# Optimization experiments

Hardware: AMD Instinct MI355X
Metric: run time of the kernel (lower is better)

## Reference

```python
import jax, jax.numpy as jnp
import numpy as np

N = 50000      # nodes (single node type 'tx')
E = 400000     # edges per edge type ('fwd' and 'rev')
F_IN = 128     # input feature dim
F = 128        # cfg.gnn.dim_inner
H = 8          # attention heads
D = F // H     # per-head dim
L = 2          # cfg.gnn.layers_mp
C = 2          # dim_out (fraud logits)


def setup_inputs() -> dict:
    key = jax.random.key(0)
    k = jax.random.split(key, 12)
    f32 = jnp.float32
    g = lambda kk, sh, fan: jax.random.normal(kk, sh, f32) / np.float32(np.sqrt(fan))
    return dict(
        x=jax.random.normal(k[0], (N, F_IN), f32),
        edge_index_fwd=jax.random.randint(k[1], (2, E), 0, N),
        edge_index_rev=jax.random.randint(k[2], (2, E), 0, N),
        in_w=g(k[3], (F_IN, F), F_IN),
        in_b=jnp.zeros((F,), f32),
        kqv_w=g(k[4], (L, F, 3 * F), F),
        kqv_b=jnp.zeros((L, 3 * F), f32),
        krel_w=g(k[5], (L, 2, H, D, D), D),
        vrel_w=g(k[6], (L, 2, H, D, D), D),
        p_rel=jnp.ones((L, 2, H), f32),
        out_w=g(k[7], (L, F, F), F),
        out_b=jnp.zeros((L, F), f32),
        skip=jnp.ones((L,), f32),
        head_w=g(k[8], (F, C), F),
        head_b=jnp.zeros((C,), f32),
    )


def reference(x, edge_index_fwd, edge_index_rev, in_w, in_b, kqv_w, kqv_b,
              krel_w, vrel_w, p_rel, out_w, out_b, skip, head_w, head_b):
    n = x.shape[0]
    ef, er = edge_index_fwd, edge_index_rev
    Ef, Er = ef.shape[1], er.shape[1]
    dst = jnp.concatenate([ef[1], er[1]])                 # [E_tot]
    scale = 1.0 / jnp.sqrt(jnp.asarray(D, x.dtype))

    h = x @ in_w + in_b                                   # in_proj['tx'], [N,F]
    for l in range(L):
        kqv = h @ kqv_w[l] + kqv_b[l]                     # [N,3F]
        k, q, v = jnp.split(kqv, 3, axis=1)
        k = k.reshape(n, H, D)
        q = q.reshape(n, H, D)
        v = v.reshape(n, H, D)
        # per-edge-type relation transforms (head-wise DxD, no bias)
        k_rel = jnp.einsum('nhd,ehdf->enhf', k, krel_w[l])  # [2,N,H,D]
        v_rel = jnp.einsum('nhd,ehdf->enhf', v, vrel_w[l])
        # gather src features per edge type, concatenate edge types
        k_j = jnp.concatenate([k_rel[0][ef[0]], k_rel[1][er[0]]], axis=0)  # [E_tot,H,D]
        v_j = jnp.concatenate([v_rel[0][ef[0]], v_rel[1][er[0]]], axis=0)
        p_e = jnp.concatenate([jnp.broadcast_to(p_rel[l, 0], (Ef, H)),
                               jnp.broadcast_to(p_rel[l, 1], (Er, H))], axis=0)
        q_i = q[dst]                                       # [E_tot,H,D]
        alpha = jnp.einsum('ehd,ehd->eh', q_i, k_j) * p_e * scale
        # segment softmax over all incoming edges of each dst node
        m = jax.ops.segment_max(alpha, dst, num_segments=n)
        ex = jnp.exp(alpha - m[dst])
        denom = jax.ops.segment_sum(ex, dst, num_segments=n)
        w = ex / (denom[dst] + 1e-16)                      # [E_tot,H]
        agg = jax.ops.segment_sum(w[:, :, None] * v_j, dst,
                                  num_segments=n).reshape(n, F)
        a = jax.nn.gelu(agg, approximate=False) @ out_w[l] + out_b[l]
        g = jax.nn.sigmoid(skip[l])
        h = jax.nn.relu(g * a + (1.0 - g) * h)             # skip + act(dropout=0)
    return h @ head_w + head_b                             # logits [N,C]
```

## Files before the change

kernel.cpp:

```cpp
#include <hip/hip_runtime.h>
#include <math.h>

typedef short short8 __attribute__((ext_vector_type(8)));
typedef float f32x4 __attribute__((ext_vector_type(4)));

#define CAP 64
#define CSTR 16

__device__ __forceinline__ unsigned short f2bf(float f){
    unsigned u = __float_as_uint(f);
    unsigned r = u + 0x7fffu + ((u >> 16) & 1u);
    return (unsigned short)(r >> 16);
}
__device__ __forceinline__ float bf2f(unsigned short s){
    return __uint_as_float((unsigned)s << 16);
}

__global__ void k_setup(const float* __restrict__ kqv_w, const float* __restrict__ kqv_b,
                        const float* __restrict__ krel_w, const float* __restrict__ vrel_w,
                        const float* __restrict__ p_rel, const float* __restrict__ out_w,
                        const float* __restrict__ out_b, const float* __restrict__ in_w,
                        const float* __restrict__ x, const float* __restrict__ head_b,
                        const int* __restrict__ ef, const int* __restrict__ er,
                        unsigned short* __restrict__ WcT, float* __restrict__ biasc,
                        unsigned short* __restrict__ WoT, float* __restrict__ biaso,
                        unsigned short* __restrict__ WiT, unsigned short* __restrict__ x16,
                        int* __restrict__ cnt, unsigned* __restrict__ srcs_pad,
                        float* __restrict__ logits, int n_nodes, int Ef, int Er)
{
    const long long E0 = Ef + Er;
    const long long N0 = E0 + 2*129*640;
    const long long N1 = N0 + 2*129*128;
    const long long N2 = N1 + 128*128;
    const long long N3 = N2 + (long long)n_nodes*32;
    const long long N4 = N3 + 2*n_nodes;

    for (long long idx = (long long)blockIdx.x*blockDim.x + threadIdx.x; idx < N4;
         idx += (long long)gridDim.x*blockDim.x) {
        if (idx < E0) {
            int e = (int)idx;
            int src, dst, tt;
            if (e < Ef) { src = ef[e]; dst = ef[Ef + e]; tt = 0; }
            else { int e2 = e - Ef; src = er[e2]; dst = er[Er + e2]; tt = 1; }
            int pos = atomicAdd(&cnt[(size_t)dst*CSTR], 1);
            if (pos < CAP)
                srcs_pad[dst*CAP + pos] = (unsigned)(tt*n_nodes + src)*32u;
        } else if (idx < N0) {
            int i = (int)(idx - E0);
            int l = i / (129*640);
            int rem = i % (129*640);
            int r = rem / 640, c = rem % 640;
            float val;
            if (c < 128) {
                val = (r < 128) ? kqv_w[((size_t)l*128 + r)*384 + 128 + c]
                                : kqv_b[l*384 + 128 + c];
            } else {
                int c2 = c - 128;
                int tt = c2 >> 8;
                int cc = c2 & 255;
                int f = cc >> 1;
                int part = cc & 1;
                int hh = f >> 4, fd = f & 15;
                const float* rw = (part == 0 ? krel_w : vrel_w)
                                  + (((size_t)(l*2 + tt)*8 + hh)*16)*16 + fd;
                int base_col = (part == 0 ? 0 : 256) + hh*16;
                float s = 0.f;
                #pragma unroll
                for (int d = 0; d < 16; ++d) {
                    float a = (r < 128) ? kqv_w[((size_t)l*128 + r)*384 + base_col + d]
                                        : kqv_b[l*384 + base_col + d];
                    s += a * rw[d*16];
                }
                if (part == 0) s *= p_rel[(l*2 + tt)*8 + hh] * 0.25f * 1.4426950408889634f;
                val = s;
            }
            if (r < 128) WcT[((size_t)l*640 + c)*128 + r] = f2bf(val);
            else         biasc[l*640 + c] = val;
        } else if (idx < N1) {
            int i = (int)(idx - N0);
            int l = i / (129*128);
            int rem = i % (129*128);
            int r = rem / 128, c = rem % 128;
            if (r < 128) WoT[((size_t)l*128 + c)*128 + r] = f2bf(out_w[((size_t)l*128 + r)*128 + c]);
            else         biaso[l*128 + c] = out_b[l*128 + c];
        } else if (idx < N2) {
            int i = (int)(idx - N1);
            int r = i >> 7, c = i & 127;
            WiT[(size_t)c*128 + r] = f2bf(in_w[(size_t)r*128 + c]);
        } else if (idx < N3) {
            long long i = idx - N2;
            float4 v = *(const float4*)&x[i*4];
            uint2 w;
            w.x = (unsigned)f2bf(v.x) | ((unsigned)f2bf(v.y) << 16);
            w.y = (unsigned)f2bf(v.z) | ((unsigned)f2bf(v.w) << 16);
            *(uint2*)&x16[i*4] = w;
        } else {
            long long i = idx - N3;
            logits[i] = head_b[i & 1];
        }
    }
}

__global__ __launch_bounds__(256) void k_mfma(
    const unsigned short* __restrict__ A16, const unsigned short* __restrict__ WT,
    const float* __restrict__ biasc, unsigned short* __restrict__ q16,
    unsigned short* __restrict__ h16, unsigned* __restrict__ kv,
    const float* __restrict__ skip, const float* __restrict__ hw,
    float* __restrict__ logits, int l,
    int n_nodes, int R, int C, int mode)
{
    __shared__ uint4 As[64*16];
    __shared__ uint4 Ws[64*16];
    int b = blockIdx.x;
    int xcd = b & 7, jj = b >> 3;
    int r_t = (jj / C)*8 + xcd;
    int c_t = jj % C;
    if (r_t >= R) return;
    int n0 = r_t*64, c0 = c_t*64;
    int t = threadIdx.x;

    #pragma unroll
    for (int it = 0; it < 4; ++it) {
        int gi = t + it*256;
        int m = gi >> 4, g = gi & 15;
        uint4 a = *(const uint4*)&A16[((size_t)(n0 + m)*16 + g)*8];
        As[m*16 + (g ^ (m & 15))] = a;
    }
    #pragma unroll
    for (int it = 0; it < 4; ++it) {
        int gi = t + it*256;
        int cw = gi >> 4, g = gi & 15;
        uint4 wv = *(const uint4*)&WT[((size_t)(c0 + cw)*16 + g)*8];
        Ws[cw*16 + (g ^ (cw & 15))] = wv;
    }
    __syncthreads();

    int lane = t & 63, w = t >> 6;
    int lm = lane & 15, quad = lane >> 4;
    f32x4 acc[4];
    #pragma unroll
    for (int i = 0; i < 4; ++i) { acc[i][0]=0.f; acc[i][1]=0.f; acc[i][2]=0.f; acc[i][3]=0.f; }

    #pragma unroll
    for (int chunk = 0; chunk < 4; ++chunk) {
        int gq = chunk*4 + quad;
        short8 bfrag = *(const short8*)&Ws[(w*16 + lm)*16 + (gq ^ lm)];
        #pragma unroll
        for (int i = 0; i < 4; ++i) {
            short8 afrag = *(const short8*)&As[(i*16 + lm)*16 + (gq ^ lm)];
            acc[i] = __builtin_amdgcn_mfma_f32_16x16x32_bf16(afrag, bfrag, acc[i], 0, 0, 0);
        }
    }

    int c = c0 + w*16 + lm;
    float bc = biasc[c];
    bool even = (lane & 1) == 0;
    if (mode == 3) {
        float g = 1.f/(1.f + expf(-skip[l]));
        float hw0 = hw[c*2], hw1 = hw[c*2 + 1];
        #pragma unroll
        for (int i = 0; i < 4; ++i) {
            #pragma unroll
            for (int rr = 0; rr < 4; ++rr) {
                int m = n0 + i*16 + quad*4 + rr;
                float nv = 0.f;
                if (m < n_nodes) {
                    float hv = bf2f(h16[(size_t)m*128 + c]);
                    nv = fmaxf(g*(acc[i][rr] + bc) + (1.f - g)*hv, 0.f);
                }
                float p0 = nv*hw0, p1 = nv*hw1;
                p0 += __shfl_xor(p0, 1); p1 += __shfl_xor(p1, 1);
                p0 += __shfl_xor(p0, 2); p1 += __shfl_xor(p1, 2);
                p0 += __shfl_xor(p0, 4); p1 += __shfl_xor(p1, 4);
                p0 += __shfl_xor(p0, 8); p1 += __shfl_xor(p1, 8);
                if (lm == 0 && m < n_nodes) {
                    atomicAdd(&logits[m*2],     p0);
                    atomicAdd(&logits[m*2 + 1], p1);
                }
            }
        }
    } else if (mode == 2) {
        float g = 1.f/(1.f + expf(-skip[l]));
        unsigned* dst = (unsigned*)h16;
        #pragma unroll
        for (int i = 0; i < 4; ++i) {
            #pragma unroll
            for (int rr = 0; rr < 4; ++rr) {
                int m = n0 + i*16 + quad*4 + rr;
                float hv = (m < n_nodes) ? bf2f(h16[(size_t)m*128 + c]) : 0.f;
                float nv = fmaxf(g*(acc[i][rr] + bc) + (1.f - g)*hv, 0.f);
                float other = __shfl_xor(nv, 1);
                if (even && m < n_nodes)
                    dst[(size_t)m*64 + (c >> 1)] =
                        (unsigned)f2bf(nv) | ((unsigned)f2bf(other) << 16);
            }
        }
    } else if (mode == 0) {
        unsigned* dst = (unsigned*)h16;
        #pragma unroll
        for (int i = 0; i < 4; ++i) {
            #pragma unroll
            for (int rr = 0; rr < 4; ++rr) {
                int m = n0 + i*16 + quad*4 + rr;
                float nv = acc[i][rr] + bc;
                float other = __shfl_xor(nv, 1);
                if (even && m < n_nodes)
                    dst[(size_t)m*64 + (c >> 1)] =
                        (unsigned)f2bf(nv) | ((unsigned)f2bf(other) << 16);
            }
        }
    } else if (c0 < 128) {
        unsigned* dst = (unsigned*)q16;
        #pragma unroll
        for (int i = 0; i < 4; ++i) {
            #pragma unroll
            for (int rr = 0; rr < 4; ++rr) {
                float val = acc[i][rr] + bc;
                float other = __shfl_xor(val, 1);
                int m = n0 + i*16 + quad*4 + rr;
                if (even && m < n_nodes)
                    dst[(size_t)m*64 + (c >> 1)] =
                        (unsigned)f2bf(val) | ((unsigned)f2bf(other) << 16);
            }
        }
    } else {
        int c2 = c - 128;
        int tt = c2 >> 8;
        int f = (c2 & 255) >> 1;
        unsigned* dst = kv + (size_t)tt*n_nodes*128;
        #pragma unroll
        for (int i = 0; i < 4; ++i) {
            #pragma unroll
            for (int rr = 0; rr < 4; ++rr) {
                float val = acc[i][rr] + bc;
                float other = __shfl_xor(val, 1);
                int m = n0 + i*16 + quad*4 + rr;
                if (even && m < n_nodes) {
                    unsigned wd = ((unsigned)f2bf(val) << 16) | (unsigned)f2bf(other);
                    dst[(size_t)m*128 + f] = wd;
                }
            }
        }
    }
}

__global__ __launch_bounds__(256) void k_attn(
    const unsigned* __restrict__ srcs_pad, const int* __restrict__ cnt,
    const uint4* __restrict__ kv, const unsigned short* __restrict__ q16,
    unsigned short* __restrict__ qa16, int n_base, int n_hi)
{
    int lane = threadIdx.x & 31;
    int n = n_base + blockIdx.x*8 + (threadIdx.x >> 5);
    if (n >= n_hi) return;
    uint2 qp = *(const uint2*)&q16[(size_t)n*128 + lane*4];
    float4 q4;
    q4.x = __uint_as_float(qp.x << 16);
    q4.y = __uint_as_float(qp.x & 0xffff0000u);
    q4.z = __uint_as_float(qp.y << 16);
    q4.w = __uint_as_float(qp.y & 0xffff0000u);
    int s = n*CAP, e = s + min(cnt[(size_t)n*CSTR], CAP);

    const uint4* kvl = kv + lane;
    const unsigned* srcs = srcs_pad;

    float lsum = 0.f;
    float4 a = make_float4(0.f, 0.f, 0.f, 0.f);

    unsigned sv0 = srcs[s],     sv1 = srcs[s + 1];
    unsigned sv2 = srcs[s + 2], sv3 = srcs[s + 3];
    uint4 w0 = kvl[sv0], w1 = kvl[sv1], w2 = kvl[sv2], w3 = kvl[sv3];

    int pos = s;

#define ATT_PAIR(wA, wB)                                                       \
    {                                                                          \
        float d0 = __uint_as_float(wA.x & 0xffff0000u)*q4.x                    \
                 + __uint_as_float(wA.y & 0xffff0000u)*q4.y                    \
                 + __uint_as_float(wA.z & 0xffff0000u)*q4.z                    \
                 + __uint_as_float(wA.w & 0xffff0000u)*q4.w;                   \
        float d1 = __uint_as_float(wB.x & 0xffff0000u)*q4.x                    \
                 + __uint_as_float(wB.y & 0xffff0000u)*q4.y                    \
                 + __uint_as_float(wB.z & 0xffff0000u)*q4.z                    \
                 + __uint_as_float(wB.w & 0xffff0000u)*q4.w;                   \
        d0 += __shfl_xor(d0, 1); d1 += __shfl_xor(d1, 1);                      \
        d0 += __shfl_xor(d0, 2); d1 += __shfl_xor(d1, 2);                      \
        float wt0 = exp2f(d0), wt1 = exp2f(d1);                                \
        lsum += wt0 + wt1;                                                     \
        a.x += wt0*__uint_as_float(wA.x << 16);                                \
        a.y += wt0*__uint_as_float(wA.y << 16);                                \
        a.z += wt0*__uint_as_float(wA.z << 16);                                \
        a.w += wt0*__uint_as_float(wA.w << 16);                                \
        a.x += wt1*__uint_as_float(wB.x << 16);                                \
        a.y += wt1*__uint_as_float(wB.y << 16);                                \
        a.z += wt1*__uint_as_float(wB.z << 16);                                \
        a.w += wt1*__uint_as_float(wB.w << 16);                                \
    }

#define ATT_ONE(wA)                                                            \
    {                                                                          \
        float d = __uint_as_float(wA.x & 0xffff0000u)*q4.x                     \
                + __uint_as_float(wA.y & 0xffff0000u)*q4.y                     \
                + __uint_as_float(wA.z & 0xffff0000u)*q4.z                     \
                + __uint_as_float(wA.w & 0xffff0000u)*q4.w;                    \
        d += __shfl_xor(d, 1);                                                 \
        d += __shfl_xor(d, 2);                                                 \
        float wt = exp2f(d);                                                   \
        lsum += wt;                                                            \
        a.x += wt*__uint_as_float(wA.x << 16);                                 \
        a.y += wt*__uint_as_float(wA.y << 16);                                 \
        a.z += wt*__uint_as_float(wA.z << 16);                                 \
        a.w += wt*__uint_as_float(wA.w << 16);                                 \
    }

    for (; pos + 3 < e; pos += 4) {
        unsigned p0 = srcs[pos + 4], p1 = srcs[pos + 5];
        ATT_PAIR(w0, w1);
        w0 = kvl[p0]; w1 = kvl[p1];
        unsigned p2 = srcs[pos + 6], p3 = srcs[pos + 7];
        ATT_PAIR(w2, w3);
        w2 = kvl[p2]; w3 = kvl[p3];
    }
    int rem = e - pos;
    if (rem > 0) {
        ATT_ONE(w0);
        if (rem > 1) ATT_ONE(w1);
        if (rem > 2) ATT_ONE(w2);
    }
#undef ATT_PAIR
#undef ATT_ONE

    float inv = 1.f/(lsum + 1e-16f);
    float x0 = a.x*inv, x1 = a.y*inv, x2 = a.z*inv, x3 = a.w*inv;
    float g0 = 0.5f*x0*(1.f + erff(x0*0.70710678118654752f));
    float g1 = 0.5f*x1*(1.f + erff(x1*0.70710678118654752f));
    float g2 = 0.5f*x2*(1.f + erff(x2*0.70710678118654752f));
    float g3 = 0.5f*x3*(1.f + erff(x3*0.70710678118654752f));
    uint2 pk;
    pk.x = (unsigned)f2bf(g0) | ((unsigned)f2bf(g1) << 16);
    pk.y = (unsigned)f2bf(g2) | ((unsigned)f2bf(g3) << 16);
    *(uint2*)&qa16[(size_t)n*128 + lane*4] = pk;
}

extern "C" void kernel_launch(void* const* d_in, const int* in_sizes, int n_in,
                              void* d_out, int out_size, void* d_ws, size_t ws_size,
                              hipStream_t stream)
{
    const float* x      = (const float*)d_in[0];
    const int*   ef     = (const int*)d_in[1];
    const int*   er     = (const int*)d_in[2];
    const float* in_w   = (const float*)d_in[3];
    const float* in_b   = (const float*)d_in[4];
    const float* kqv_w  = (const float*)d_in[5];
    const float* kqv_b  = (const float*)d_in[6];
    const float* krel_w = (const float*)d_in[7];
    const float* vrel_w = (const float*)d_in[8];
    const float* p_rel  = (const float*)d_in[9];
    const float* out_w  = (const float*)d_in[10];
    const float* out_b  = (const float*)d_in[11];
    const float* skip   = (const float*)d_in[12];
    const float* head_w = (const float*)d_in[13];
    const float* head_b = (const float*)d_in[14];
    float* out = (float*)d_out;

    int n_nodes = in_sizes[0] / 128;
    int Ef = in_sizes[1] / 2, Er = in_sizes[2] / 2;
    int ntile = (n_nodes + 63)/64;
    int npad = ntile*64;

    float* p = (float*)d_ws;
    unsigned* kv = (unsigned*)p; p += (size_t)2*n_nodes*128;
    unsigned short* h16  = (unsigned short*)p; p += (size_t)npad*128/2;
    unsigned short* q16  = (unsigned short*)p; p += (size_t)npad*128/2;
    unsigned short* qa16 = (unsigned short*)p; p += (size_t)npad*128/2;
    unsigned short* x16  = (unsigned short*)p; p += (size_t)npad*128/2;
    unsigned short* WiT = (unsigned short*)p; p += (size_t)(128*128)/2;
    unsigned short* WcT = (unsigned short*)p; p += (size_t)(2*640*128)/2;
    float* biasc = p; p += 2*640;
    unsigned short* WoT = (unsigned short*)p; p += (size_t)(2*128*128)/2;
    float* biaso = p; p += 2*128;
    int* cnt = (int*)p;            p += (size_t)n_nodes*CSTR;
    unsigned* srcs_pad = (unsigned*)p; p += (size_t)n_nodes*CAP;

    int Rg = (ntile + 7)/8;

    hipMemsetAsync(cnt, 0, (size_t)n_nodes*CSTR*sizeof(int), stream);
    hipMemsetAsync(srcs_pad, 0, (size_t)n_nodes*CAP*sizeof(unsigned), stream);
    k_setup<<<7500, 256, 0, stream>>>(kqv_w, kqv_b, krel_w, vrel_w, p_rel, out_w, out_b,
                                      in_w, x, head_b, ef, er, WcT, biasc, WoT, biaso,
                                      WiT, x16, cnt, srcs_pad, out, n_nodes, Ef, Er);

    int nh = (((n_nodes + 1)/2) + 7) & ~7;
    if (nh > n_nodes) nh = n_nodes;

    k_mfma<<<Rg*8*2, 256, 0, stream>>>(x16, WiT, in_b, nullptr, h16, kv, skip,
                                       head_w, out, 0, n_nodes, ntile, 2, 0);
    for (int l = 0; l < 2; ++l) {
        k_mfma<<<Rg*8*10, 256, 0, stream>>>(h16, WcT + (size_t)l*640*128,
                                            biasc + l*640, q16, nullptr, kv, skip,
                                            head_w, out, l, n_nodes, ntile, 10, 1);
        k_attn<<<nh/8, 256, 0, stream>>>(srcs_pad, cnt, (const uint4*)kv, q16, qa16,
                                         0, nh);
        k_attn<<<(n_nodes - nh + 7)/8, 256, 0, stream>>>(srcs_pad, cnt, (const uint4*)kv,
                                                         q16, qa16, nh, n_nodes);
        int omode = (l == 1) ? 3 : 2;
        k_mfma<<<Rg*8*2, 256, 0, stream>>>(qa16, WoT + (size_t)l*128*128,
                                           biaso + l*128, nullptr, h16, kv, skip,
                                           head_w, out, l, n_nodes, ntile, 2, omode);
    }
}
```

Baseline: 394.5 us.

## Partition edge bucketing by XCD so each die handles its own destination range

```diff
diff --git a/kernel.cpp b/kernel.cpp
--- a/kernel.cpp
+++ b/kernel.cpp
@@ -6,6 +6,7 @@
 
 #define CAP 64
 #define CSTR 16
+#define ECHUNK 2048
 
 __device__ __forceinline__ unsigned short f2bf(float f){
     unsigned u = __float_as_uint(f);
@@ -26,10 +27,38 @@
                         unsigned short* __restrict__ WoT, float* __restrict__ biaso,
                         unsigned short* __restrict__ WiT, unsigned short* __restrict__ x16,
                         int* __restrict__ cnt, unsigned* __restrict__ srcs_pad,
-                        float* __restrict__ logits, int n_nodes, int Ef, int Er)
+                        int* __restrict__ q, float* __restrict__ logits,
+                        int n_nodes, int Ef, int Er, int rng, int nchk)
 {
-    const long long E0 = Ef + Er;
-    const long long N0 = E0 + 2*129*640;
+    int Etot = Ef + Er;
+    int xcd;
+    asm volatile("s_getreg_b32 %0, hwreg(HW_REG_XCC_ID)" : "=s"(xcd));
+    xcd &= 7;
+    int lo = xcd * rng;
+    int m = min(rng, n_nodes - lo);
+    __shared__ int s_chunk;
+    while (true) {
+        if (threadIdx.x == 0) s_chunk = atomicAdd(&q[xcd*16], 1);
+        __syncthreads();
+        int c = s_chunk;
+        __syncthreads();
+        if (c >= nchk) break;
+        int base = c*ECHUNK;
+        int end = min(base + ECHUNK, Etot);
+        for (int e = base + (int)threadIdx.x; e < end; e += 256) {
+            int src, dst, tt;
+            if (e < Ef) { src = ef[e]; dst = ef[Ef + e]; tt = 0; }
+            else { int e2 = e - Ef; src = er[e2]; dst = er[Er + e2]; tt = 1; }
+            unsigned r = (unsigned)(dst - lo);
+            if (r < (unsigned)m) {
+                int pos = atomicAdd(&cnt[(size_t)dst*CSTR], 1);
+                if (pos < CAP)
+                    srcs_pad[dst*CAP + pos] = (unsigned)(tt*n_nodes + src)*32u;
+            }
+        }
+    }
+
+    const long long N0 = 2*129*640;
     const long long N1 = N0 + 2*129*128;
     const long long N2 = N1 + 128*128;
     const long long N3 = N2 + (long long)n_nodes*32;
@@ -37,16 +66,8 @@
 
     for (long long idx = (long long)blockIdx.x*blockDim.x + threadIdx.x; idx < N4;
          idx += (long long)gridDim.x*blockDim.x) {
-        if (idx < E0) {
-            int e = (int)idx;
-            int src, dst, tt;
-            if (e < Ef) { src = ef[e]; dst = ef[Ef + e]; tt = 0; }
-            else { int e2 = e - Ef; src = er[e2]; dst = er[Er + e2]; tt = 1; }
-            int pos = atomicAdd(&cnt[(size_t)dst*CSTR], 1);
-            if (pos < CAP)
-                srcs_pad[dst*CAP + pos] = (unsigned)(tt*n_nodes + src)*32u;
-        } else if (idx < N0) {
-            int i = (int)(idx - E0);
+        if (idx < N0) {
+            int i = (int)idx;
             int l = i / (129*640);
             int rem = i % (129*640);
             int r = rem / 640, c = rem % 640;
@@ -364,6 +385,7 @@
 
     int n_nodes = in_sizes[0] / 128;
     int Ef = in_sizes[1] / 2, Er = in_sizes[2] / 2;
+    int Etot = Ef + Er;
     int ntile = (n_nodes + 63)/64;
     int npad = ntile*64;
 
@@ -379,15 +401,19 @@
     unsigned short* WoT = (unsigned short*)p; p += (size_t)(2*128*128)/2;
     float* biaso = p; p += 2*128;
     int* cnt = (int*)p;            p += (size_t)n_nodes*CSTR;
+    int* q   = (int*)p;            p += 8*16;
     unsigned* srcs_pad = (unsigned*)p; p += (size_t)n_nodes*CAP;
 
     int Rg = (ntile + 7)/8;
-
-    hipMemsetAsync(cnt, 0, (size_t)n_nodes*CSTR*sizeof(int), stream);
+    int rng = (n_nodes + 7)/8;
+    int nchk = (Etot + ECHUNK - 1)/ECHUNK;
+
+    hipMemsetAsync(cnt, 0, ((size_t)n_nodes*CSTR + 8*16)*sizeof(int), stream);
     hipMemsetAsync(srcs_pad, 0, (size_t)n_nodes*CAP*sizeof(unsigned), stream);
     k_setup<<<7500, 256, 0, stream>>>(kqv_w, kqv_b, krel_w, vrel_w, p_rel, out_w, out_b,
                                       in_w, x, head_b, ef, er, WcT, biasc, WoT, biaso,
-                                      WiT, x16, cnt, srcs_pad, out, n_nodes, Ef, Er);
+                                      WiT, x16, cnt, srcs_pad, q, out,
+                                      n_nodes, Ef, Er, rng, nchk);
 
     int nh = (((n_nodes + 1)/2) + 7) & ~7;
     if (nh > n_nodes) nh = n_nodes;
```

Result: no change. 400.1 us (+1.4%).
